# Kernel tuning notes

Measured on AMD Instinct MI355X. Metric: run time of the kernel, lower is better.

## Reference

```python
import jax, jax.numpy as jnp
import numpy as np
from jax.scipy.linalg import expm

DIM = 128
BF = 2          # branching_factor
H = 8           # num_heads
MAX_DEPTH = 12
PAD = BF + 1    # padding value used by pad_sequence in the torch module
N = 256         # number of positions


def setup_inputs() -> dict:
    key = jax.random.key(0)
    k1, k2 = jax.random.split(key)
    # raw _primitives parameter (the torch init applies softmax+cumsum to rand;
    # any values work for the math -- only the skew-hermitian part matters)
    prim = jax.random.uniform(k1, (BF * H + 1, DIM, DIM), dtype=jnp.float32)
    positions = jax.random.randint(k2, (N,), 0, BF ** MAX_DEPTH)  # node indices, >= 0
    return {"primitives_param": prim, "positions": positions}


def _path_words(positions):
    """Vectorized equivalent of create_paths + pad_sequence.

    For node index n the branch path is built by walking up the tree:
    branch = (n-1) % BF, parent = (n-1) // BF. Digits come out leaf->root,
    so we reverse the valid prefix and right-pad with PAD to MAX_DEPTH.
    """
    d = positions.astype(jnp.int32)
    digs = []
    for _ in range(MAX_DEPTH):
        valid = d > 0
        digs.append(jnp.where(valid, (d - 1) % BF, PAD))
        d = jnp.where(valid, (d - 1) // BF, 0)
    R = jnp.stack(digs, axis=1)            # (N, 12) leaf->root digits
    depth = jnp.sum(R != PAD, axis=1)       # path length per token
    idx = depth[:, None] - 1 - jnp.arange(MAX_DEPTH)[None, :]
    pw = jnp.take_along_axis(R, jnp.clip(idx, 0, MAX_DEPTH - 1), axis=1)
    pw = jnp.where(idx >= 0, pw, PAD)       # (N, 12) root->leaf, PAD-padded
    return pw, depth


def reference(primitives_param, positions):
    pw, depth = _path_words(positions)

    # ---- steps matrix (tree distance), mirrors the no_grad block ----
    pm = pw != PAD                                        # (N, 12)
    mask = pm[:, None, :] & pm[None, :, :]                # (N, N, 12)
    eq = pw[:, None, :] == pw[None, :, :]
    common = jnp.cumprod(eq.astype(jnp.int32), axis=-1).astype(bool) & mask
    cpl = common.sum(-1)                                  # common prefix length
    steps = depth[:, None] + depth[None, :] - 2 * cpl     # (N, N) int

    # ---- unitary primitives: expm of the skew(-hermitian, real) part ----
    skew = primitives_param - jnp.swapaxes(primitives_param, -1, -2)
    prims = expm(skew)                                    # (BF*H+1, DIM, DIM)
    sos = prims[-1]
    P = prims[:-1].reshape(BF, H, DIM, DIM)

    n_tok = pw.shape[0]
    maps = jnp.broadcast_to(jnp.eye(DIM, dtype=prims.dtype)[None, None],
                            (n_tok, H, DIM, DIM))
    sos_ptr = pw[:, 0] == -1                              # never true for pos>=0, kept for fidelity
    maps = jnp.where(sos_ptr[:, None, None, None], sos[None, None], maps)

    # fused gather-indexed scan over tree depth: instead of BF masked matmuls
    # per depth, gather each token's branch primitive and do one batched matmul.
    for d in range(MAX_DEPTH):
        sel = pw[:, d]                                    # (N,) in {0..BF-1} or PAD
        Pk = P[jnp.clip(sel, 0, BF - 1)]                  # (N, H, DIM, DIM)
        new = jnp.einsum('nhij,nhjk->nhik', maps, Pk)
        maps = jnp.where((sel < BF)[:, None, None, None], new, maps)

    return maps, steps
```

## Files before the change

kernel.cpp:

```cpp
#include <hip/hip_runtime.h>

typedef unsigned short ushort_t;
typedef unsigned int uint_t;
typedef __attribute__((ext_vector_type(8))) short bf16x8;
typedef __attribute__((ext_vector_type(4))) float f32x4;

#define NMAT 16
#define MSZ 16384
#define NTAB 30

__device__ __forceinline__ ushort_t f32_bf16(float f) {
  uint_t u = __builtin_bit_cast(uint_t, f);
  u += 0x7FFFu + ((u >> 16) & 1u);
  return (ushort_t)(u >> 16);
}

__device__ __forceinline__ float bf16_f32(ushort_t b) {
  uint_t u = ((uint_t)b) << 16;
  return __builtin_bit_cast(float, u);
}

__device__ __forceinline__ int swz(int r, int k) {
  return r * 128 + (((k >> 3) ^ (r & 7)) << 3) + (k & 7);
}

__device__ __forceinline__ int tab_off(int L) {
  return (L == 1) ? 0 : (L == 2) ? 2 : (L == 3) ? 6 : 14;
}

__device__ __forceinline__ void mm_frag(const ushort_t* U, const ushort_t* V,
                                        int r0, int c0, int quad, int l16,
                                        f32x4 (&acc)[4][4]) {
#pragma unroll
  for (int rt = 0; rt < 4; rt++)
#pragma unroll
    for (int ct = 0; ct < 4; ct++) {
      f32x4 z = {0.f, 0.f, 0.f, 0.f};
      acc[rt][ct] = z;
    }
#pragma unroll
  for (int kt = 0; kt < 4; kt++) {
    int k = kt * 32 + quad * 8;
    bf16x8 a[4], b[4];
#pragma unroll
    for (int rt = 0; rt < 4; rt++) a[rt] = *(const bf16x8*)(&U[swz(r0 + rt * 16 + l16, k)]);
#pragma unroll
    for (int ct = 0; ct < 4; ct++) b[ct] = *(const bf16x8*)(&V[swz(c0 + ct * 16 + l16, k)]);
#pragma unroll
    for (int rt = 0; rt < 4; rt++)
#pragma unroll
      for (int ct = 0; ct < 4; ct++)
        acc[rt][ct] = __builtin_amdgcn_mfma_f32_16x16x32_bf16(a[rt], b[ct], acc[rt][ct], 0, 0, 0);
  }
}

__device__ __forceinline__ void store_T(ushort_t* dst, const f32x4 (&acc)[4][4],
                                        int r0, int c0, int quad, int l16,
                                        float scale, float cdiag) {
#pragma unroll
  for (int rt = 0; rt < 4; rt++)
#pragma unroll
    for (int ct = 0; ct < 4; ct++) {
      int dr = r0 + rt * 16 + quad * 4, dc = c0 + ct * 16 + l16;
      float v[4];
#pragma unroll
      for (int i = 0; i < 4; i++) {
        v[i] = scale * acc[rt][ct][i];
        if (dr + i == dc) v[i] += cdiag;
      }
      uint2 pk;
      pk.x = (uint_t)f32_bf16(v[0]) | ((uint_t)f32_bf16(v[1]) << 16);
      pk.y = (uint_t)f32_bf16(v[2]) | ((uint_t)f32_bf16(v[3]) << 16);
      *(uint2*)(&dst[swz(dc, dr)]) = pk;
    }
}

__device__ __forceinline__ void set_ident(ushort_t* dst, int t, float c) {
  ushort_t cb = f32_bf16(c);
  for (int i = 0; i < 64; i++) {
    int e = i * 256 + t;
    int r = e >> 7, k = e & 127;
    dst[swz(r, k)] = (r == k) ? cb : (ushort_t)0;
  }
}

__global__ __launch_bounds__(256, 1) void expm1_kernel(const float* __restrict__ prim,
                                                       ushort_t* __restrict__ wsCS) {
  __shared__ ushort_t __align__(16) bufA[MSZ];
  __shared__ ushort_t __align__(16) bufB[MSZ];
  int kmat = blockIdx.x >> 1, which = blockIdx.x & 1;
  int t = threadIdx.x, wave = t >> 6, lane = t & 63;
  int quad = lane >> 4, l16 = lane & 15;
  int r0 = (wave >> 1) * 64, c0 = (wave & 1) * 64;
  const float* p = prim + kmat * MSZ;

  for (int i = 0; i < 64; i++) {
    int e = i * 256 + t;
    int r = e >> 7, c = e & 127;
    bufA[swz(r, c)] = f32_bf16((p[r * 128 + c] - p[c * 128 + r]) * 0.125f);
  }
  __syncthreads();

  f32x4 acc[4][4];
  mm_frag(bufA, bufA, r0, c0, quad, l16, acc);
  __syncthreads();
  store_T(bufB, acc, r0, c0, quad, l16, -1.f, 0.f);
  __syncthreads();

  uint2 yv[4][4];
#pragma unroll
  for (int rt = 0; rt < 4; rt++)
#pragma unroll
    for (int ct = 0; ct < 4; ct++) {
      int dr = r0 + rt * 16 + quad * 4, dc = c0 + ct * 16 + l16;
      yv[rt][ct] = *(const uint2*)(&bufB[swz(dc, dr)]);
    }

  mm_frag(bufB, bufB, r0, c0, quad, l16, acc);
  __syncthreads();
  store_T(bufB, acc, r0, c0, quad, l16, 1.f, 0.f);

  float coef[9];
  if (which == 0) {
    coef[0] = 1.f; coef[1] = 1.f / 2; coef[2] = 1.f / 24; coef[3] = 1.f / 720;
    coef[4] = 1.f / 40320; coef[5] = 1.f / 3628800.f; coef[6] = 1.f / 479001600.f;
    coef[7] = 1.f / 87178291200.f; coef[8] = 1.f / 20922789888000.f;
  } else {
    coef[0] = 1.f; coef[1] = 1.f / 6; coef[2] = 1.f / 120; coef[3] = 1.f / 5040;
    coef[4] = 1.f / 362880.f; coef[5] = 1.f / 39916800.f; coef[6] = 1.f / 6227020800.f;
    coef[7] = 1.f / 1307674368000.f; coef[8] = 1.f / 355687428096000.f;
  }

  set_ident(bufA, t, coef[8]);
  __syncthreads();

#pragma unroll
  for (int k = 3; k >= 0; k--) {
    mm_frag(bufB, bufA, r0, c0, quad, l16, acc);
    __syncthreads();
    float cd = coef[2 * k], cy = coef[2 * k + 1];
#pragma unroll
    for (int rt = 0; rt < 4; rt++)
#pragma unroll
      for (int ct = 0; ct < 4; ct++) {
        int dr = r0 + rt * 16 + quad * 4, dc = c0 + ct * 16 + l16;
        uint2 yp = yv[rt][ct];
        float y[4] = {bf16_f32((ushort_t)(yp.x & 0xffff)), bf16_f32((ushort_t)(yp.x >> 16)),
                      bf16_f32((ushort_t)(yp.y & 0xffff)), bf16_f32((ushort_t)(yp.y >> 16))};
        float v[4];
#pragma unroll
        for (int i = 0; i < 4; i++) {
          v[i] = acc[rt][ct][i] + cy * y[i];
          if (dr + i == dc) v[i] += cd;
        }
        uint2 pk;
        pk.x = (uint_t)f32_bf16(v[0]) | ((uint_t)f32_bf16(v[1]) << 16);
        pk.y = (uint_t)f32_bf16(v[2]) | ((uint_t)f32_bf16(v[3]) << 16);
        *(uint2*)(&bufA[swz(dc, dr)]) = pk;
      }
    __syncthreads();
  }
  ushort_t* dst = wsCS + (size_t)(which * NMAT + kmat) * MSZ;
  for (int i = 0; i < 8; i++) {
    int e = (i * 256 + t) * 8;
    int r = e >> 7, k = e & 127;
    *(uint4*)(dst + e) = *(const uint4*)(&bufA[swz(r, k)]);
  }
}

__global__ __launch_bounds__(256, 1) void expm2_kernel(
    const float* __restrict__ prim, const ushort_t* __restrict__ wsCS,
    ushort_t* __restrict__ TN, ushort_t* __restrict__ TT) {
  __shared__ ushort_t __align__(16) bufA[MSZ];
  __shared__ ushort_t __align__(16) bufB[MSZ];
  int kmat = blockIdx.x;
  int t = threadIdx.x, wave = t >> 6, lane = t & 63;
  int quad = lane >> 4, l16 = lane & 15;
  int r0 = (wave >> 1) * 64, c0 = (wave & 1) * 64;
  const float* p = prim + kmat * MSZ;
  const ushort_t* Cg = wsCS + (size_t)kmat * MSZ;
  const ushort_t* Sg = wsCS + (size_t)(NMAT + kmat) * MSZ;

  for (int i = 0; i < 64; i++) {
    int e = i * 256 + t;
    int r = e >> 7, c = e & 127;
    bufA[swz(r, c)] = f32_bf16((p[r * 128 + c] - p[c * 128 + r]) * 0.125f);
  }
  for (int i = 0; i < 8; i++) {
    int e = (i * 256 + t) * 8;
    int r = e >> 7, k = e & 127;
    *(uint4*)(&bufB[swz(r, k)]) = *(const uint4*)(Sg + e);
  }
  __syncthreads();

  f32x4 acc[4][4];
  mm_frag(bufA, bufB, r0, c0, quad, l16, acc);
  __syncthreads();
#pragma unroll
  for (int rt = 0; rt < 4; rt++)
#pragma unroll
    for (int ct = 0; ct < 4; ct++) {
      int dr = r0 + rt * 16 + quad * 4, dc = c0 + ct * 16 + l16;
      uint2 cp = *(const uint2*)(Cg + dc * 128 + dr);
      float cf[4] = {bf16_f32((ushort_t)(cp.x & 0xffff)), bf16_f32((ushort_t)(cp.x >> 16)),
                     bf16_f32((ushort_t)(cp.y & 0xffff)), bf16_f32((ushort_t)(cp.y >> 16))};
      uint2 en, et;
      en.x = (uint_t)f32_bf16(cf[0] - acc[rt][ct][0]) | ((uint_t)f32_bf16(cf[1] - acc[rt][ct][1]) << 16);
      en.y = (uint_t)f32_bf16(cf[2] - acc[rt][ct][2]) | ((uint_t)f32_bf16(cf[3] - acc[rt][ct][3]) << 16);
      et.x = (uint_t)f32_bf16(cf[0] + acc[rt][ct][0]) | ((uint_t)f32_bf16(cf[1] + acc[rt][ct][1]) << 16);
      et.y = (uint_t)f32_bf16(cf[2] + acc[rt][ct][2]) | ((uint_t)f32_bf16(cf[3] + acc[rt][ct][3]) << 16);
      *(uint2*)(&bufA[swz(dc, dr)]) = en;
      *(uint2*)(&bufB[swz(dc, dr)]) = et;
    }
  __syncthreads();

#pragma unroll 1
  for (int sq = 0; sq < 3; sq++) {
    mm_frag(bufA, bufB, r0, c0, quad, l16, acc);
    __syncthreads();
#pragma unroll
    for (int rt = 0; rt < 4; rt++)
#pragma unroll
      for (int ct = 0; ct < 4; ct++) {
        int dr = r0 + rt * 16 + quad * 4, dc = c0 + ct * 16 + l16;
        uint2 pk;
        pk.x = (uint_t)f32_bf16(acc[rt][ct][0]) | ((uint_t)f32_bf16(acc[rt][ct][1]) << 16);
        pk.y = (uint_t)f32_bf16(acc[rt][ct][2]) | ((uint_t)f32_bf16(acc[rt][ct][3]) << 16);
        *(uint2*)(&bufB[swz(dc, dr)]) = pk;
#pragma unroll
        for (int i = 0; i < 4; i++) bufA[swz(dr + i, dc)] = f32_bf16(acc[rt][ct][i]);
      }
    __syncthreads();
  }
  for (int i = 0; i < 8; i++) {
    int e = (i * 256 + t) * 8;
    int r = e >> 7, k = e & 127;
    *(uint4*)(TN + (size_t)kmat * MSZ + e) = *(const uint4*)(&bufA[swz(r, k)]);
    *(uint4*)(TT + (size_t)kmat * MSZ + e) = *(const uint4*)(&bufB[swz(r, k)]);
  }
}

__global__ __launch_bounds__(256) void table_kernel(ushort_t* __restrict__ TN,
                                                    ushort_t* __restrict__ TT, int mode) {
  int bx = blockIdx.x;
  int eA, eB, eO, h;
  if (mode == 0) {
    int c = bx >> 3; h = bx & 7;
    eA = c >> 1; eB = c & 1; eO = 2 + c;
  } else {
    if (bx < 64) {
      int c = bx >> 3; h = bx & 7;
      eA = 2 + (c >> 1); eB = c & 1; eO = 6 + c;
    } else {
      int c = (bx - 64) >> 3; h = (bx - 64) & 7;
      eA = 2 + (c >> 2); eB = 2 + (c & 3); eO = 14 + c;
    }
  }
  int t = threadIdx.x, wave = t >> 6, lane = t & 63;
  int quad = lane >> 4, l16 = lane & 15;
  int r0 = (wave >> 1) * 64, c0 = (wave & 1) * 64;
  const ushort_t* A = TN + ((size_t)eA * 8 + h) * MSZ;
  const ushort_t* B = TT + ((size_t)eB * 8 + h) * MSZ;
  ushort_t* oN = TN + ((size_t)eO * 8 + h) * MSZ;
  ushort_t* oT = TT + ((size_t)eO * 8 + h) * MSZ;

  bf16x8 a[4][4], b[4][4];
#pragma unroll
  for (int kt = 0; kt < 4; kt++) {
#pragma unroll
    for (int rt = 0; rt < 4; rt++)
      a[kt][rt] = *(const bf16x8*)(A + (r0 + rt * 16 + l16) * 128 + kt * 32 + quad * 8);
#pragma unroll
    for (int ct = 0; ct < 4; ct++)
      b[kt][ct] = *(const bf16x8*)(B + (c0 + ct * 16 + l16) * 128 + kt * 32 + quad * 8);
  }
  f32x4 acc[4][4];
#pragma unroll
  for (int rt = 0; rt < 4; rt++)
#pragma unroll
    for (int ct = 0; ct < 4; ct++) {
      f32x4 z = {0.f, 0.f, 0.f, 0.f};
      acc[rt][ct] = z;
    }
#pragma unroll
  for (int kt = 0; kt < 4; kt++)
#pragma unroll
    for (int rt = 0; rt < 4; rt++)
#pragma unroll
      for (int ct = 0; ct < 4; ct++)
        acc[rt][ct] = __builtin_amdgcn_mfma_f32_16x16x32_bf16(a[kt][rt], b[kt][ct], acc[rt][ct], 0, 0, 0);
#pragma unroll
  for (int rt = 0; rt < 4; rt++)
#pragma unroll
    for (int ct = 0; ct < 4; ct++) {
      int dr = r0 + rt * 16 + quad * 4, dc = c0 + ct * 16 + l16;
      uint2 pk;
      pk.x = (uint_t)f32_bf16(acc[rt][ct][0]) | ((uint_t)f32_bf16(acc[rt][ct][1]) << 16);
      pk.y = (uint_t)f32_bf16(acc[rt][ct][2]) | ((uint_t)f32_bf16(acc[rt][ct][3]) << 16);
      *(uint2*)(oT + dc * 128 + dr) = pk;
#pragma unroll
      for (int i = 0; i < 4; i++) oN[(dr + i) * 128 + dc] = f32_bf16(acc[rt][ct][i]);
    }
}

__global__ void steps_kernel(const int* __restrict__ pos, float* __restrict__ os, int N) {
  int i = blockIdx.x, j = threadIdx.x;
  int mi = pos[i] + 1, mj = pos[j] + 1;
  int di = 31 - __builtin_clz((unsigned)mi);
  int dj = 31 - __builtin_clz((unsigned)mj);
  int tt = di < dj ? di : dj;
  unsigned x = (unsigned)((mi >> (di - tt)) ^ (mj >> (dj - tt)));
  int cpl = tt - (x ? (32 - __builtin_clz(x)) : 0);
  os[i * N + j] = (float)(di + dj - 2 * cpl);
}

__global__ __launch_bounds__(256, 4) void maps_kernel(
    const ushort_t* __restrict__ TN, const ushort_t* __restrict__ TT,
    const int* __restrict__ positions, float* __restrict__ out) {
  __shared__ ushort_t __align__(16) Mb[MSZ];
  int bx = blockIdx.x;
  int n = bx >> 3, h = bx & 7;
  int t = threadIdx.x, wave = t >> 6, lane = t & 63;
  int quad = lane >> 4, l16 = lane & 15;
  int m = positions[n] + 1;
  int depth = 31 - __builtin_clz((unsigned)m);
  float* ob = out + (size_t)(n * 8 + h) * MSZ;

  if (depth == 0) {
    for (int i = 0; i < 64; i++) {
      int e = i * 256 + t;
      int r = e >> 7, k = e & 127;
      ob[e] = (r == k) ? 1.0f : 0.0f;
    }
    return;
  }
  if (depth <= 4) {
    int c = m & ((1 << depth) - 1);
    const ushort_t* src = TN + ((size_t)(tab_off(depth) + c) * 8 + h) * MSZ;
    for (int i = 0; i < 8; i++) {
      int e = (i * 256 + t) * 8;
      bf16x8 v = *(const bf16x8*)(src + e);
      f32x4 lo = {bf16_f32((ushort_t)v[0]), bf16_f32((ushort_t)v[1]),
                  bf16_f32((ushort_t)v[2]), bf16_f32((ushort_t)v[3])};
      f32x4 hi = {bf16_f32((ushort_t)v[4]), bf16_f32((ushort_t)v[5]),
                  bf16_f32((ushort_t)v[6]), bf16_f32((ushort_t)v[7])};
      *(f32x4*)(ob + e) = lo;
      *(f32x4*)(ob + e + 4) = hi;
    }
    return;
  }

  int K = (depth + 3) >> 2;
  int L0 = depth - 4 * (K - 1);
  int c0v = (m >> (depth - L0)) & ((1 << L0) - 1);
  const ushort_t* src0 = TN + ((size_t)(tab_off(L0) + c0v) * 8 + h) * MSZ;

  int r0 = (wave >> 1) * 64, c0 = (wave & 1) * 64;
#pragma unroll
  for (int i = 0; i < 8; i++) {
    int e = (i * 256 + t) * 8;
    int r = e >> 7, k = e & 127;
    *(uint4*)(&Mb[swz(r, k)]) = *(const uint4*)(src0 + e);
  }
  __syncthreads();

  int rem = depth - L0;
  while (rem > 0) {
    int cb = (m >> (rem - 4)) & 15;
    const ushort_t* Ap = TT + ((size_t)(14 + cb) * 8 + h) * MSZ;
    f32x4 acc[4][4];
#pragma unroll
    for (int rt = 0; rt < 4; rt++)
#pragma unroll
      for (int ct = 0; ct < 4; ct++) {
        f32x4 z = {0.f, 0.f, 0.f, 0.f};
        acc[rt][ct] = z;
      }
#pragma unroll
    for (int kt = 0; kt < 4; kt++) {
      int k = kt * 32 + quad * 8;
      bf16x8 a[4], b[4];
#pragma unroll
      for (int rt = 0; rt < 4; rt++)
        a[rt] = *(const bf16x8*)(Ap + (r0 + rt * 16 + l16) * 128 + k);
#pragma unroll
      for (int ct = 0; ct < 4; ct++) b[ct] = *(const bf16x8*)(&Mb[swz(c0 + ct * 16 + l16, k)]);
#pragma unroll
      for (int rt = 0; rt < 4; rt++)
#pragma unroll
        for (int ct = 0; ct < 4; ct++)
          acc[rt][ct] = __builtin_amdgcn_mfma_f32_16x16x32_bf16(a[rt], b[ct], acc[rt][ct], 0, 0, 0);
    }
    rem -= 4;
    if (rem == 0) {
#pragma unroll
      for (int rt = 0; rt < 4; rt++)
#pragma unroll
        for (int ct = 0; ct < 4; ct++) {
          int dr = r0 + rt * 16 + quad * 4;
          int dc = c0 + ct * 16 + l16;
          *(f32x4*)(ob + dc * 128 + dr) = acc[rt][ct];
        }
    } else {
      __syncthreads();
#pragma unroll
      for (int rt = 0; rt < 4; rt++)
#pragma unroll
        for (int ct = 0; ct < 4; ct++) {
          int dr = r0 + rt * 16 + quad * 4;
          int dc = c0 + ct * 16 + l16;
          uint2 pk;
          pk.x = (uint_t)f32_bf16(acc[rt][ct][0]) | ((uint_t)f32_bf16(acc[rt][ct][1]) << 16);
          pk.y = (uint_t)f32_bf16(acc[rt][ct][2]) | ((uint_t)f32_bf16(acc[rt][ct][3]) << 16);
          *(uint2*)(&Mb[swz(dc, dr)]) = pk;
        }
      __syncthreads();
    }
  }
}

extern "C" void kernel_launch(void* const* d_in, const int* in_sizes, int n_in,
                              void* d_out, int out_size, void* d_ws, size_t ws_size,
                              hipStream_t stream) {
  const float* prim = (const float*)d_in[0];
  const int* positions = (const int*)d_in[1];
  int N = in_sizes[1];
  float* out = (float*)d_out;

  ushort_t* wsCS = (ushort_t*)d_ws;
  ushort_t* TN = wsCS + (size_t)2 * NMAT * MSZ;
  ushort_t* TT = TN + (size_t)NTAB * 8 * MSZ;

  steps_kernel<<<N, N, 0, stream>>>(positions, out + (size_t)N * 8 * MSZ, N);
  expm1_kernel<<<2 * NMAT, 256, 0, stream>>>(prim, wsCS);
  expm2_kernel<<<NMAT, 256, 0, stream>>>(prim, wsCS, TN, TT);
  table_kernel<<<32, 256, 0, stream>>>(TN, TT, 0);
  table_kernel<<<192, 256, 0, stream>>>(TN, TT, 1);
  maps_kernel<<<N * 8, 256, 0, stream>>>(TN, TT, positions, out);
}
```

Before: 235.2 us.

## Unroll maps_kernel chain into two fixed stages with prefetched A operands

Replaces the generic while-loop over 4-level table multiplies with an explicit one- or two-stage sequence (depth up to 12). All A-operand fragments for a stage are loaded from global memory into registers up front, and the first stage's A loads are issued before the initial barrier so they overlap the shared-memory fill. A second shared buffer removes the barrier that the old single-buffer write-back needed. The cost is 64KB of LDS per block, more registers for the prefetched fragments, and launch bounds lowered from 4 to 2 blocks per CU, which reduces occupancy.

```diff
diff --git a/kernel.cpp b/kernel.cpp
--- a/kernel.cpp
+++ b/kernel.cpp
@@ -314,10 +314,10 @@
   os[i * N + j] = (float)(di + dj - 2 * cpl);
 }
 
-__global__ __launch_bounds__(256, 4) void maps_kernel(
+__global__ __launch_bounds__(256, 2) void maps_kernel(
     const ushort_t* __restrict__ TN, const ushort_t* __restrict__ TT,
     const int* __restrict__ positions, float* __restrict__ out) {
-  __shared__ ushort_t __align__(16) Mb[MSZ];
+  __shared__ ushort_t __align__(16) Mb[2][MSZ];
   int bx = blockIdx.x;
   int n = bx >> 3, h = bx & 7;
   int t = threadIdx.x, wave = t >> 6, lane = t & 63;
@@ -354,21 +354,68 @@
   int L0 = depth - 4 * (K - 1);
   int c0v = (m >> (depth - L0)) & ((1 << L0) - 1);
   const ushort_t* src0 = TN + ((size_t)(tab_off(L0) + c0v) * 8 + h) * MSZ;
+  bool two = (K == 3);
+  int c1 = (m >> (4 * (K - 2))) & 15;
+  int c2 = m & 15;
+  const ushort_t* Ap1 = TT + ((size_t)(14 + c1) * 8 + h) * MSZ;
+  const ushort_t* Ap2 = TT + ((size_t)(14 + c2) * 8 + h) * MSZ;
 
   int r0 = (wave >> 1) * 64, c0 = (wave & 1) * 64;
 #pragma unroll
   for (int i = 0; i < 8; i++) {
     int e = (i * 256 + t) * 8;
     int r = e >> 7, k = e & 127;
-    *(uint4*)(&Mb[swz(r, k)]) = *(const uint4*)(src0 + e);
-  }
-  __syncthreads();
-
-  int rem = depth - L0;
-  while (rem > 0) {
-    int cb = (m >> (rem - 4)) & 15;
-    const ushort_t* Ap = TT + ((size_t)(14 + cb) * 8 + h) * MSZ;
-    f32x4 acc[4][4];
+    *(uint4*)(&Mb[0][swz(r, k)]) = *(const uint4*)(src0 + e);
+  }
+  bf16x8 a1[4][4];
+#pragma unroll
+  for (int kt = 0; kt < 4; kt++)
+#pragma unroll
+    for (int rt = 0; rt < 4; rt++)
+      a1[kt][rt] = *(const bf16x8*)(Ap1 + (r0 + rt * 16 + l16) * 128 + kt * 32 + quad * 8);
+  __syncthreads();
+
+  f32x4 acc[4][4];
+#pragma unroll
+  for (int rt = 0; rt < 4; rt++)
+#pragma unroll
+    for (int ct = 0; ct < 4; ct++) {
+      f32x4 z = {0.f, 0.f, 0.f, 0.f};
+      acc[rt][ct] = z;
+    }
+#pragma unroll
+  for (int kt = 0; kt < 4; kt++) {
+    int k = kt * 32 + quad * 8;
+    bf16x8 b[4];
+#pragma unroll
+    for (int ct = 0; ct < 4; ct++) b[ct] = *(const bf16x8*)(&Mb[0][swz(c0 + ct * 16 + l16, k)]);
+#pragma unroll
+    for (int rt = 0; rt < 4; rt++)
+#pragma unroll
+      for (int ct = 0; ct < 4; ct++)
+        acc[rt][ct] = __builtin_amdgcn_mfma_f32_16x16x32_bf16(a1[kt][rt], b[ct], acc[rt][ct], 0, 0, 0);
+  }
+
+  if (two) {
+    bf16x8 a2[4][4];
+#pragma unroll
+    for (int kt = 0; kt < 4; kt++)
+#pragma unroll
+      for (int rt = 0; rt < 4; rt++)
+        a2[kt][rt] = *(const bf16x8*)(Ap2 + (r0 + rt * 16 + l16) * 128 + kt * 32 + quad * 8);
+#pragma unroll
+    for (int rt = 0; rt < 4; rt++)
+#pragma unroll
+      for (int ct = 0; ct < 4; ct++) {
+        int dr = r0 + rt * 16 + quad * 4;
+        int dc = c0 + ct * 16 + l16;
+        uint2 pk;
+        pk.x = (uint_t)f32_bf16(acc[rt][ct][0]) | ((uint_t)f32_bf16(acc[rt][ct][1]) << 16);
+        pk.y = (uint_t)f32_bf16(acc[rt][ct][2]) | ((uint_t)f32_bf16(acc[rt][ct][3]) << 16);
+        *(uint2*)(&Mb[1][swz(dc, dr)]) = pk;
+      }
+    __syncthreads();
+
 #pragma unroll
     for (int rt = 0; rt < 4; rt++)
 #pragma unroll
@@ -379,44 +426,25 @@
 #pragma unroll
     for (int kt = 0; kt < 4; kt++) {
       int k = kt * 32 + quad * 8;
-      bf16x8 a[4], b[4];
+      bf16x8 b[4];
+#pragma unroll
+      for (int ct = 0; ct < 4; ct++) b[ct] = *(const bf16x8*)(&Mb[1][swz(c0 + ct * 16 + l16, k)]);
 #pragma unroll
       for (int rt = 0; rt < 4; rt++)
-        a[rt] = *(const bf16x8*)(Ap + (r0 + rt * 16 + l16) * 128 + k);
-#pragma unroll
-      for (int ct = 0; ct < 4; ct++) b[ct] = *(const bf16x8*)(&Mb[swz(c0 + ct * 16 + l16, k)]);
-#pragma unroll
-      for (int rt = 0; rt < 4; rt++)
 #pragma unroll
         for (int ct = 0; ct < 4; ct++)
-          acc[rt][ct] = __builtin_amdgcn_mfma_f32_16x16x32_bf16(a[rt], b[ct], acc[rt][ct], 0, 0, 0);
-    }
-    rem -= 4;
-    if (rem == 0) {
-#pragma unroll
-      for (int rt = 0; rt < 4; rt++)
-#pragma unroll
-        for (int ct = 0; ct < 4; ct++) {
-          int dr = r0 + rt * 16 + quad * 4;
-          int dc = c0 + ct * 16 + l16;
-          *(f32x4*)(ob + dc * 128 + dr) = acc[rt][ct];
-        }
-    } else {
-      __syncthreads();
-#pragma unroll
-      for (int rt = 0; rt < 4; rt++)
-#pragma unroll
-        for (int ct = 0; ct < 4; ct++) {
-          int dr = r0 + rt * 16 + quad * 4;
-          int dc = c0 + ct * 16 + l16;
-          uint2 pk;
-          pk.x = (uint_t)f32_bf16(acc[rt][ct][0]) | ((uint_t)f32_bf16(acc[rt][ct][1]) << 16);
-          pk.y = (uint_t)f32_bf16(acc[rt][ct][2]) | ((uint_t)f32_bf16(acc[rt][ct][3]) << 16);
-          *(uint2*)(&Mb[swz(dc, dr)]) = pk;
-        }
-      __syncthreads();
-    }
-  }
+          acc[rt][ct] = __builtin_amdgcn_mfma_f32_16x16x32_bf16(a2[kt][rt], b[ct], acc[rt][ct], 0, 0, 0);
+    }
+  }
+
+#pragma unroll
+  for (int rt = 0; rt < 4; rt++)
+#pragma unroll
+    for (int ct = 0; ct < 4; ct++) {
+      int dr = r0 + rt * 16 + quad * 4;
+      int dc = c0 + ct * 16 + l16;
+      *(f32x4*)(ob + dc * 128 + dr) = acc[rt][ct];
+    }
 }
 
 extern "C" void kernel_launch(void* const* d_in, const int* in_sizes, int n_in,
```

Measured after the change: 221.4 us (median of 2 runs). 5.9% less time.
